# Optimization experiments

Hardware: AMD Instinct MI355X
Metric: run time of the kernel (lower is better)

The kernel has to match this reference:

```python
import jax, jax.numpy as jnp
import numpy as np

THETA = 10000.0
AXES_DIM = (16, 56, 56)  # sums to head_dim=128
HEADS = 24
HEAD_DIM = 128
EPS = 1e-5


def _pos_embed(ids):
    # ids: (S, n_axes) int -> cos, sin each (S, head_dim//2)
    pos = ids.astype(jnp.float32)
    cos_out, sin_out = [], []
    for i, d in enumerate(AXES_DIM):
        freqs = 1.0 / (THETA ** (jnp.arange(0, d, 2, dtype=jnp.float32) / d))  # (d/2,)
        ang = pos[:, i][:, None] * freqs[None, :]  # (S, d/2)
        cos_out.append(jnp.cos(ang))
        sin_out.append(jnp.sin(ang))
    return jnp.concatenate(cos_out, -1), jnp.concatenate(sin_out, -1)


def _rms_norm(x, w):
    # per-head RMSNorm over last dim (head_dim)
    var = jnp.mean(x * x, axis=-1, keepdims=True)
    return x * jax.lax.rsqrt(var + EPS) * w


def _apply_rope(x, cos, sin):
    # non-neox (interleaved) rotary. x: (B,S,H,D), cos/sin: (S,D/2)
    x1 = x[..., 0::2]
    x2 = x[..., 1::2]
    c = cos[None, :, None, :]
    s = sin[None, :, None, :]
    o1 = x1 * c - x2 * s
    o2 = x2 * c + x1 * s
    return jnp.stack([o1, o2], axis=-1).reshape(x.shape)


def setup_inputs() -> dict:
    key = jax.random.key(0)
    ks = jax.random.split(key, 12)
    B, S_img, S_txt, D = 1, 2048, 512, 3072
    sd = 1.0 / np.sqrt(D)
    return {
        "hidden_states": jax.random.normal(ks[0], (B, S_img, D), jnp.float32),
        "encoder_hidden_states": jax.random.normal(ks[1], (B, S_txt, D), jnp.float32),
        "ids": jax.random.randint(ks[2], (S_txt + S_img, 3), 0, 64, jnp.int32),
        "w_qkv": jax.random.normal(ks[3], (D, 3 * D), jnp.float32) * sd,
        "w_add_qkv": jax.random.normal(ks[4], (D, 3 * D), jnp.float32) * sd,
        "b_add_qkv": jax.random.normal(ks[5], (3 * D,), jnp.float32) * 0.02,
        "w_out": jax.random.normal(ks[6], (D, D), jnp.float32) * sd,
        "b_out": jax.random.normal(ks[7], (D,), jnp.float32) * 0.02,
        "w_add_out": jax.random.normal(ks[8], (D, D), jnp.float32) * sd,
        "b_add_out": jax.random.normal(ks[9], (D,), jnp.float32) * 0.02,
        "norm_q_w": jnp.ones((HEAD_DIM,), jnp.float32),
        "norm_k_w": jnp.ones((HEAD_DIM,), jnp.float32),
        "norm_add_q_w": jnp.ones((HEAD_DIM,), jnp.float32),
        "norm_add_k_w": jnp.ones((HEAD_DIM,), jnp.float32),
    }


def reference(hidden_states, encoder_hidden_states, ids, w_qkv, w_add_qkv,
              b_add_qkv, w_out, b_out, w_add_out, b_add_out,
              norm_q_w, norm_k_w, norm_add_q_w, norm_add_k_w):
    B, S_img, D = hidden_states.shape
    S_txt = encoder_hidden_states.shape[1]
    H, Dh = HEADS, HEAD_DIM

    # fused QKV projections
    qkv = hidden_states @ w_qkv  # (B, S_img, 3D)
    q, k, v = jnp.split(qkv, 3, axis=-1)
    q = _rms_norm(q.reshape(B, S_img, H, Dh), norm_q_w)
    k = _rms_norm(k.reshape(B, S_img, H, Dh), norm_k_w)
    v = v.reshape(B, S_img, H, Dh)

    eqkv = encoder_hidden_states @ w_add_qkv + b_add_qkv
    eq, ek, ev = jnp.split(eqkv, 3, axis=-1)
    eq = _rms_norm(eq.reshape(B, S_txt, H, Dh), norm_add_q_w)
    ek = _rms_norm(ek.reshape(B, S_txt, H, Dh), norm_add_k_w)
    ev = ev.reshape(B, S_txt, H, Dh)

    # joint sequence: text first, then image
    q = jnp.concatenate([eq, q], axis=1)
    k = jnp.concatenate([ek, k], axis=1)
    v = jnp.concatenate([ev, v], axis=1)

    # multi-axis RoPE over joint positions
    cos, sin = _pos_embed(ids)  # (S_txt+S_img, Dh/2)
    q = _apply_rope(q, cos, sin)
    k = _apply_rope(k, cos, sin)

    # scaled dot-product attention (non-causal)
    scale = 1.0 / np.sqrt(Dh)
    scores = jnp.einsum("bqhd,bkhd->bhqk", q, k) * scale
    probs = jax.nn.softmax(scores, axis=-1)
    attn = jnp.einsum("bhqk,bkhd->bqhd", probs, v)
    attn = attn.reshape(B, S_txt + S_img, H * Dh)

    enc_out = attn[:, :S_txt] @ w_add_out + b_add_out
    img_out = attn[:, S_txt:] @ w_out + b_out
    return img_out, enc_out
```

## Files before the change

kernel.cpp:

```cpp
#include <hip/hip_runtime.h>

typedef __attribute__((ext_vector_type(8))) short short8;
typedef __attribute__((ext_vector_type(4))) short short4v;
typedef __attribute__((ext_vector_type(4))) float floatx4;

__device__ __forceinline__ float b2f(short b) {
  union { unsigned u; float f; } v; v.u = ((unsigned)(unsigned short)b) << 16; return v.f;
}
__device__ __forceinline__ short f2b(float f) {
  union { float f; unsigned u; } v; v.f = f;
  return (short)((v.u + 0x7fffu + ((v.u >> 16) & 1u)) >> 16);
}
__device__ __forceinline__ unsigned cvtpk(float lo, float hi) {
  unsigned r;
  asm("v_cvt_pk_bf16_f32 %0, %1, %2" : "=v"(r) : "v"(lo), "v"(hi));
  return r;
}
__device__ __forceinline__ float loadf(const void* p, size_t i, bool f32) {
  return f32 ? ((const float*)p)[i] : b2f(((const short*)p)[i]);
}
__device__ __forceinline__ short8 load8(const void* p, size_t i, bool f32) {
  if (f32) {
    const float* fp = (const float*)p + i;
    float4 a = *(const float4*)fp;
    float4 b = *(const float4*)(fp + 4);
    short8 r;
    r[0] = f2b(a.x); r[1] = f2b(a.y); r[2] = f2b(a.z); r[3] = f2b(a.w);
    r[4] = f2b(b.x); r[5] = f2b(b.y); r[6] = f2b(b.z); r[7] = f2b(b.w);
    return r;
  }
  return *(const short8*)((const short*)p + i);
}

__device__ __forceinline__ void gload16(const short* g, short* l) {
  __builtin_amdgcn_global_load_lds(
      (const __attribute__((address_space(1))) unsigned int*)g,
      (__attribute__((address_space(3))) unsigned int*)l, 16, 0, 0);
}

__global__ void detect_dtype(const unsigned short* __restrict__ w, int* __restrict__ flag) {
  __shared__ int cnt;
  if (threadIdx.x == 0) cnt = 0;
  __syncthreads();
  int bad = 0;
  for (int i = threadIdx.x; i < 4096; i += 256) {
    int e = (w[i] >> 7) & 0xFF;
    if (e >= 0xC8) bad++;
  }
  atomicAdd(&cnt, bad);
  __syncthreads();
  if (threadIdx.x == 0) *flag = (cnt > 64) ? 1 : 0;
}

__global__ __launch_bounds__(256)
void cvt_bf16_2(const void* __restrict__ srcA, long n8A,
                const void* __restrict__ srcB, long n8B,
                short* __restrict__ dst, const int* __restrict__ dflag) {
  const bool f32 = (*dflag != 0);
  const long n8 = n8A + n8B;
  long stride = (long)gridDim.x * 256;
  for (long i = (long)blockIdx.x * 256 + threadIdx.x; i < n8; i += stride) {
    const void* s; long e;
    if (i < n8A) { s = srcA; e = i * 8; } else { s = srcB; e = (i - n8A) * 8; }
    if (f32) {
      const float* fp = (const float*)s + e;
      float4 a = *(const float4*)fp;
      float4 b = *(const float4*)(fp + 4);
      short8 r;
      r[0] = f2b(a.x); r[1] = f2b(a.y); r[2] = f2b(a.z); r[3] = f2b(a.w);
      r[4] = f2b(b.x); r[5] = f2b(b.y); r[6] = f2b(b.z); r[7] = f2b(b.w);
      *(short8*)(dst + i * 8) = r;
    } else {
      *(short8*)(dst + i * 8) = *(const short8*)((const short*)s + e);
    }
  }
}

__global__ __launch_bounds__(256)
void cvt_tw(const void* __restrict__ wq, short* __restrict__ wqd,
            const void* __restrict__ waq, short* __restrict__ waqd,
            const void* __restrict__ wo, short* __restrict__ wod,
            const void* __restrict__ wao, short* __restrict__ waod,
            const int* __restrict__ dflag) {
  __shared__ short st[64][72];
  const bool f32 = (*dflag != 0);
  const int K = 3072;
  int b = blockIdx.x;
  const void* src; short* dst; int N, n0, k0;
  if (b < 13824) {
    src = (b < 6912) ? wq : waq;
    dst = (b < 6912) ? wqd : waqd;
    int rem = b % 6912;
    N = 9216; n0 = (rem % 144) << 6; k0 = (rem / 144) << 6;
  } else {
    b -= 13824;
    src = (b < 2304) ? wo : wao;
    dst = (b < 2304) ? wod : waod;
    int rem = b % 2304;
    N = 3072; n0 = (rem % 48) << 6; k0 = (rem / 48) << 6;
  }
  const int c4 = threadIdx.x & 15;
  const int rq = threadIdx.x >> 4;
#pragma unroll
  for (int r = 0; r < 4; ++r) {
    int k = r * 16 + rq;
    int n = c4 * 4;
    short v0, v1, v2, v3;
    if (f32) {
      const float* sp = (const float*)src + (size_t)(k0 + k) * N + n0 + n;
      float4 f = *(const float4*)sp;
      v0 = f2b(f.x); v1 = f2b(f.y); v2 = f2b(f.z); v3 = f2b(f.w);
    } else {
      const short* sp = (const short*)src + (size_t)(k0 + k) * N + n0 + n;
      short4v s = *(const short4v*)sp;
      v0 = s[0]; v1 = s[1]; v2 = s[2]; v3 = s[3];
    }
    st[n + 0][k] = v0; st[n + 1][k] = v1; st[n + 2][k] = v2; st[n + 3][k] = v3;
  }
  __syncthreads();
  const int n = threadIdx.x >> 2;
  const int kc = (threadIdx.x & 3) << 4;
  short8 a = *(const short8*)(&st[n][kc]);
  short8 bb = *(const short8*)(&st[n][kc + 8]);
  short* dp = dst + (size_t)(n0 + n) * K + k0 + kc;
  *(short8*)(dp) = a;
  *(short8*)(dp + 8) = bb;
}

__global__ __launch_bounds__(256, 2)
void gemm_bt(const void* __restrict__ A, int a_row0,
             const void* __restrict__ B, const void* __restrict__ bias,
             void* __restrict__ C, int c_row0, int N, int K,
             const int* __restrict__ dflag, int aIn, int cOut) {
  __shared__ short As[128 * 32];
  __shared__ short Bs[128 * 32];
  const bool f32 = (*dflag != 0);
  const bool a32 = aIn && f32;
  const bool c32 = cOut && f32;
  const int tid = threadIdx.x;
  const int lane = tid & 63, w = tid >> 6;
  const int wm = w & 1, wn = w >> 1;
  const int qg = lane >> 4, l16 = lane & 15;
  const int m0 = blockIdx.y << 7, n0 = blockIdx.x << 7;

  const int arow = tid >> 2, ak = (tid & 3) << 3;
  const int brow = tid >> 4, bc = (tid & 15) << 3;
  const int rot = tid & 15;

  floatx4 acc[4][4];
#pragma unroll
  for (int i = 0; i < 4; ++i)
#pragma unroll
    for (int j = 0; j < 4; ++j) acc[i][j] = (floatx4){0.f, 0.f, 0.f, 0.f};

  for (int k0 = 0; k0 < K; k0 += 32) {
    __syncthreads();
#pragma unroll
    for (int j = 0; j < 2; ++j) {
      short8 av = load8(A, (size_t)(a_row0 + m0 + j * 64 + arow) * K + (k0 + ak), a32);
      *(short8*)(As + (j * 64 + arow) * 32 + ak) = av;
      int kr = j * 16 + brow;
      short8 bv = load8(B, (size_t)(k0 + kr) * N + (n0 + bc), f32);
      int kq = kr >> 3, kj = kr & 7;
#pragma unroll
      for (int s = 0; s < 8; ++s) {
        int u = (s + rot) & 7;
        int n = bc + u;
        Bs[(n << 5) + ((kq ^ (n & 3)) << 3) + kj] = bv[u];
      }
    }
    __syncthreads();
    short8 a[4];
#pragma unroll
    for (int mi = 0; mi < 4; ++mi)
      a[mi] = *(const short8*)(As + (wm * 64 + mi * 16 + l16) * 32 + qg * 8);
#pragma unroll
    for (int ni = 0; ni < 4; ++ni) {
      int n = wn * 64 + ni * 16 + l16;
      short8 b = *(const short8*)(Bs + (n << 5) + ((qg ^ (n & 3)) << 3));
#pragma unroll
      for (int mi = 0; mi < 4; ++mi)
        acc[mi][ni] = __builtin_amdgcn_mfma_f32_16x16x32_bf16(a[mi], b, acc[mi][ni], 0, 0, 0);
    }
  }
#pragma unroll
  for (int ni = 0; ni < 4; ++ni) {
    int col = n0 + wn * 64 + ni * 16 + l16;
    float bv = bias ? loadf(bias, col, f32) : 0.0f;
#pragma unroll
    for (int mi = 0; mi < 4; ++mi) {
      int row = m0 + wm * 64 + mi * 16 + qg * 4;
#pragma unroll
      for (int r = 0; r < 4; ++r) {
        size_t idx = (size_t)(c_row0 + row + r) * N + col;
        float val = acc[mi][ni][r] + bv;
        if (c32) ((float*)C)[idx] = val;
        else     ((short*)C)[idx] = f2b(val);
      }
    }
  }
}

__global__ __launch_bounds__(256, 2)
void gemm_bf2(const short* __restrict__ A,
              const short* __restrict__ BTa, const void* __restrict__ biasa,
              int a0a, int c0a, int nYa,
              const short* __restrict__ BTb, const void* __restrict__ biasb,
              int a0b, int c0b,
              void* __restrict__ C, int N, int K,
              const int* __restrict__ dflag, int cOut) {
  __shared__ short Ls[3 * 8192 + 3 * 4096];
#define ASB(b) (Ls + (b) * 8192)
#define BSB(b) (Ls + 24576 + (b) * 4096)
  const bool f32 = (*dflag != 0);
  const bool c32 = cOut && f32;
  const int bx = blockIdx.x;
  const int y = blockIdx.y;
  const short* BT; const void* bias; int arow0, crow0;
  if (y < nYa) { BT = BTa; bias = biasa; arow0 = a0a + (y << 8); crow0 = c0a + (y << 8); }
  else { int my = y - nYa; BT = BTb; bias = biasb; arow0 = a0b + (my << 8); crow0 = c0b + (my << 8); }
  const int tid = threadIdx.x;
  const int lane = tid & 63, w = tid >> 6;
  const int wm = w & 1, wn = w >> 1;
  const int qg = lane >> 4, l16 = lane & 15;
  const int n0 = bx << 7;
  const int garow = lane >> 2;
  const int gcir = lane & 3;
  const int nk = K >> 5;
  const int swz = (gcir ^ (garow & 3) ^ (garow >> 2)) << 3;
  const short* Abase = A + (size_t)(arow0 + w * 64 + garow) * K + swz;
  const short* Bbase = BT + (size_t)(n0 + w * 32 + garow) * K + swz;
  const int rswz = (l16 & 3) ^ (l16 >> 2);

  floatx4 acc[8][4];
#pragma unroll
  for (int i = 0; i < 8; ++i)
#pragma unroll
    for (int j = 0; j < 4; ++j) acc[i][j] = (floatx4){0.f, 0.f, 0.f, 0.f};

  auto STAGE = [&](int buf, int k0) {
#pragma unroll
    for (int j = 0; j < 4; ++j)
      gload16(Abase + (size_t)j * 16 * K + k0, ASB(buf) + ((w * 4 + j) << 9));
#pragma unroll
    for (int j = 0; j < 2; ++j)
      gload16(Bbase + (size_t)j * 16 * K + k0, BSB(buf) + ((w * 2 + j) << 9));
  };

  STAGE(0, 0);
  if (nk > 1) STAGE(1, 32);

  int cb = 0;
  for (int t = 0; t < nk; ++t) {
    if (t + 1 < nk) {
      asm volatile("s_waitcnt vmcnt(6) lgkmcnt(0)" ::: "memory");
    } else {
      asm volatile("s_waitcnt vmcnt(0) lgkmcnt(0)" ::: "memory");
    }
    __builtin_amdgcn_s_barrier();
    if (t + 2 < nk) {
      int sb = (cb == 0) ? 2 : cb - 1;
      STAGE(sb, (t + 2) << 5);
    }
    short8 a[8], b[4];
#pragma unroll
    for (int mi = 0; mi < 8; ++mi) {
      int ra = wm * 128 + mi * 16 + l16;
      a[mi] = *(const short8*)(ASB(cb) + (ra << 5) + ((qg ^ rswz) << 3));
    }
#pragma unroll
    for (int ni = 0; ni < 4; ++ni) {
      int n = wn * 64 + ni * 16 + l16;
      b[ni] = *(const short8*)(BSB(cb) + (n << 5) + ((qg ^ rswz) << 3));
    }
    __builtin_amdgcn_s_setprio(1);
#pragma unroll
    for (int ni = 0; ni < 4; ++ni)
#pragma unroll
      for (int mi = 0; mi < 8; ++mi)
        acc[mi][ni] = __builtin_amdgcn_mfma_f32_16x16x32_bf16(a[mi], b[ni], acc[mi][ni], 0, 0, 0);
    __builtin_amdgcn_s_setprio(0);
    cb = (cb == 2) ? 0 : cb + 1;
  }
  __builtin_amdgcn_s_barrier();
  if (!c32) {
    short* wreg = Ls + w * 4096;
#pragma unroll
    for (int half = 0; half < 2; ++half) {
#pragma unroll
      for (int ni = 0; ni < 4; ++ni) {
        float bvv = bias ? loadf(bias, n0 + wn * 64 + ni * 16 + l16, f32) : 0.0f;
#pragma unroll
        for (int mi2 = 0; mi2 < 4; ++mi2)
#pragma unroll
          for (int r = 0; r < 4; ++r)
            wreg[(mi2 * 16 + qg * 4 + r) * 64 + ni * 16 + l16] =
                f2b(acc[half * 4 + mi2][ni][r] + bvv);
      }
      asm volatile("s_waitcnt lgkmcnt(0)" ::: "memory");
#pragma unroll
      for (int j = 0; j < 8; ++j) {
        int row = j * 8 + (lane >> 3);
        int col = (lane & 7) * 8;
        short8 v = *(const short8*)(wreg + row * 64 + col);
        *(short8*)((short*)C + (size_t)(crow0 + wm * 128 + half * 64 + row) * N +
                   n0 + wn * 64 + col) = v;
      }
      asm volatile("s_waitcnt lgkmcnt(0)" ::: "memory");
    }
  } else {
    float* wregf = (float*)(Ls) + w * 2048;
#pragma unroll
    for (int half = 0; half < 2; ++half) {
#pragma unroll
      for (int ch = 0; ch < 2; ++ch) {
#pragma unroll
        for (int nh = 0; nh < 2; ++nh) {
          int ni = ch * 2 + nh;
          float bvv = bias ? loadf(bias, n0 + wn * 64 + ni * 16 + l16, f32) : 0.0f;
#pragma unroll
          for (int mi2 = 0; mi2 < 4; ++mi2)
#pragma unroll
            for (int r = 0; r < 4; ++r)
              wregf[(mi2 * 16 + qg * 4 + r) * 32 + nh * 16 + l16] =
                  acc[half * 4 + mi2][ni][r] + bvv;
        }
        asm volatile("s_waitcnt lgkmcnt(0)" ::: "memory");
#pragma unroll
        for (int j = 0; j < 8; ++j) {
          int row = j * 8 + (lane >> 3);
          int c4 = (lane & 7) * 4;
          float4 v = *(const float4*)(wregf + row * 32 + c4);
          *(float4*)((float*)C + (size_t)(crow0 + wm * 128 + half * 64 + row) * N +
                     n0 + wn * 64 + ch * 32 + c4) = v;
        }
        asm volatile("s_waitcnt lgkmcnt(0)" ::: "memory");
      }
    }
  }
#undef ASB
#undef BSB
}

__global__ __launch_bounds__(256, 3)
void gemm_bf128(const short* __restrict__ A,
                const short* __restrict__ BTa, const void* __restrict__ biasa,
                int a0a, int c0a, int nYa,
                const short* __restrict__ BTb, const void* __restrict__ biasb,
                int a0b, int c0b,
                void* __restrict__ C, int N, int K,
                const int* __restrict__ dflag, int cOut) {
  __shared__ short Ls[6 * 128 * 32];
#define ASB(b) (Ls + (b) * 4096)
#define BSB(b) (Ls + (3 + (b)) * 4096)
  const bool f32 = (*dflag != 0);
  const bool c32 = cOut && f32;
  const int bx = blockIdx.x;
  const int y = blockIdx.y;
  const short* BT; const void* bias; int arow0, crow0;
  if (y < nYa) { BT = BTa; bias = biasa; arow0 = a0a + (y << 7); crow0 = c0a + (y << 7); }
  else { int my = y - nYa; BT = BTb; bias = biasb; arow0 = a0b + (my << 7); crow0 = c0b + (my << 7); }
  const int tid = threadIdx.x;
  const int lane = tid & 63, w = tid >> 6;
  const int wm = w & 1, wn = w >> 1;
  const int qg = lane >> 4, l16 = lane & 15;
  const int n0 = bx << 7;
  const int garow = lane >> 2;
  const int gcir = lane & 3;
  const int nk = K >> 5;
  const int swz = (gcir ^ (garow & 3) ^ (garow >> 2)) << 3;
  const short* Abase = A + (size_t)(arow0 + w * 32 + garow) * K + swz;
  const short* Bbase = BT + (size_t)(n0 + w * 32 + garow) * K + swz;
  const int rswz = (l16 & 3) ^ (l16 >> 2);

  floatx4 acc[4][4];
#pragma unroll
  for (int i = 0; i < 4; ++i)
#pragma unroll
    for (int j = 0; j < 4; ++j) acc[i][j] = (floatx4){0.f, 0.f, 0.f, 0.f};

  auto STAGE = [&](int buf, int k0) {
#pragma unroll
    for (int j = 0; j < 2; ++j) {
      gload16(Abase + (size_t)j * 16 * K + k0, ASB(buf) + ((w * 2 + j) << 9));
      gload16(Bbase + (size_t)j * 16 * K + k0, BSB(buf) + ((w * 2 + j) << 9));
    }
  };

  STAGE(0, 0);
  if (nk > 1) STAGE(1, 32);

  int cb = 0;
  for (int t = 0; t < nk; ++t) {
    if (t + 1 < nk) {
      asm volatile("s_waitcnt vmcnt(4) lgkmcnt(0)" ::: "memory");
    } else {
      asm volatile("s_waitcnt vmcnt(0) lgkmcnt(0)" ::: "memory");
    }
    __builtin_amdgcn_s_barrier();
    if (t + 2 < nk) {
      int sb = (cb == 0) ? 2 : cb - 1;
      STAGE(sb, (t + 2) << 5);
    }
    short8 a[4], b[4];
#pragma unroll
    for (int mi = 0; mi < 4; ++mi) {
      int ra = wm * 64 + mi * 16 + l16;
      a[mi] = *(const short8*)(ASB(cb) + (ra << 5) + ((qg ^ rswz) << 3));
    }
#pragma unroll
    for (int ni = 0; ni < 4; ++ni) {
      int n = wn * 64 + ni * 16 + l16;
      b[ni] = *(const short8*)(BSB(cb) + (n << 5) + ((qg ^ rswz) << 3));
    }
    __builtin_amdgcn_s_setprio(1);
#pragma unroll
    for (int ni = 0; ni < 4; ++ni)
#pragma unroll
      for (int mi = 0; mi < 4; ++mi)
        acc[mi][ni] = __builtin_amdgcn_mfma_f32_16x16x32_bf16(a[mi], b[ni], acc[mi][ni], 0, 0, 0);
    __builtin_amdgcn_s_setprio(0);
    cb = (cb == 2) ? 0 : cb + 1;
  }
  __builtin_amdgcn_s_barrier();
  if (!c32) {
    short* wreg = Ls + w * 4096;
#pragma unroll
    for (int ni = 0; ni < 4; ++ni) {
      float bvv = bias ? loadf(bias, n0 + wn * 64 + ni * 16 + l16, f32) : 0.0f;
#pragma unroll
      for (int mi = 0; mi < 4; ++mi)
#pragma unroll
        for (int r = 0; r < 4; ++r)
          wreg[(mi * 16 + qg * 4 + r) * 64 + ni * 16 + l16] = f2b(acc[mi][ni][r] + bvv);
    }
    asm volatile("s_waitcnt lgkmcnt(0)" ::: "memory");
#pragma unroll
    for (int j = 0; j < 8; ++j) {
      int row = j * 8 + (lane >> 3);
      int col = (lane & 7) * 8;
      short8 v = *(const short8*)(wreg + row * 64 + col);
      *(short8*)((short*)C + (size_t)(crow0 + wm * 64 + row) * N + n0 + wn * 64 + col) = v;
    }
  } else {
    float* wregf = (float*)(Ls) + w * 2048;
#pragma unroll
    for (int half = 0; half < 2; ++half) {
#pragma unroll
      for (int nh = 0; nh < 2; ++nh) {
        int ni = half * 2 + nh;
        float bvv = bias ? loadf(bias, n0 + wn * 64 + ni * 16 + l16, f32) : 0.0f;
#pragma unroll
        for (int mi = 0; mi < 4; ++mi)
#pragma unroll
          for (int r = 0; r < 4; ++r)
            wregf[(mi * 16 + qg * 4 + r) * 32 + nh * 16 + l16] = acc[mi][ni][r] + bvv;
      }
      asm volatile("s_waitcnt lgkmcnt(0)" ::: "memory");
#pragma unroll
      for (int j = 0; j < 8; ++j) {
        int row = j * 8 + (lane >> 3);
        int c4 = (lane & 7) * 4;
        float4 v = *(const float4*)(wregf + row * 32 + c4);
        *(float4*)((float*)C + (size_t)(crow0 + wm * 64 + row) * N + n0 + wn * 64 + half * 32 + c4) = v;
      }
      asm volatile("s_waitcnt lgkmcnt(0)" ::: "memory");
    }
  }
#undef ASB
#undef BSB
}

__global__ __launch_bounds__(512)
void norm_rope(short* __restrict__ qkv, const int* __restrict__ ids,
               const void* __restrict__ nqw, const void* __restrict__ nkw,
               const void* __restrict__ naqw, const void* __restrict__ nakw,
               const int* __restrict__ dflag) {
  const bool f32 = (*dflag != 0);
  const int t = blockIdx.x, wv = threadIdx.x >> 6, lane = threadIdx.x & 63;
  const bool txt = t < 512;
  int p = lane, axis; float expo;
  if (p < 8)       { axis = 0; expo = (float)(2 * p) * (1.0f / 16.0f); }
  else if (p < 36) { axis = 1; expo = (float)(2 * (p - 8)) * (1.0f / 56.0f); }
  else             { axis = 2; expo = (float)(2 * (p - 36)) * (1.0f / 56.0f); }
  float freq = __expf(-expo * 9.210340371976184f);
  float ang = (float)ids[t * 3 + axis] * freq;
  float s, c; sincosf(ang, &s, &c);
  const void* qw = txt ? naqw : nqw;
  const void* kw = txt ? nakw : nkw;
  float w0q = loadf(qw, 2 * lane, f32), w1q = loadf(qw, 2 * lane + 1, f32);
  float w0k = loadf(kw, 2 * lane, f32), w1k = loadf(kw, 2 * lane + 1, f32);
  const float QS = 0.08838834764831845f * 1.4426950408889634f;
#pragma unroll
  for (int i = 0; i < 3; ++i) {
    int h = wv + 8 * i;
    short* qp = qkv + (size_t)t * 9216 + h * 128 + 2 * lane;
    short* kp = qp + 3072;
    union { unsigned u; short sh[2]; } qv, kv;
    qv.u = *(const unsigned*)qp;
    kv.u = *(const unsigned*)kp;
    float q0 = b2f(qv.sh[0]), q1 = b2f(qv.sh[1]);
    float k0 = b2f(kv.sh[0]), k1 = b2f(kv.sh[1]);
    float sq = q0 * q0 + q1 * q1, sk = k0 * k0 + k1 * k1;
#pragma unroll
    for (int o = 1; o < 64; o <<= 1) { sq += __shfl_xor(sq, o); sk += __shfl_xor(sk, o); }
    float rq = rsqrtf(sq * (1.0f / 128.0f) + 1e-5f);
    float rk = rsqrtf(sk * (1.0f / 128.0f) + 1e-5f);
    float qn0 = q0 * rq * w0q, qn1 = q1 * rq * w1q;
    float kn0 = k0 * rk * w0k, kn1 = k1 * rk * w1k;
    float qo0 = qn0 * c - qn1 * s, qo1 = qn1 * c + qn0 * s;
    float ko0 = kn0 * c - kn1 * s, ko1 = kn1 * c + kn0 * s;
    union { unsigned u; short sh[2]; } qo, ko;
    qo.sh[0] = f2b(qo0 * QS);
    qo.sh[1] = f2b(qo1 * QS);
    ko.sh[0] = f2b(ko0); ko.sh[1] = f2b(ko1);
    *(unsigned*)qp = qo.u;
    *(unsigned*)kp = ko.u;
  }
}

__global__ __launch_bounds__(512, 2)
void attn_fa(const short* __restrict__ qkv, short* __restrict__ attn) {
  __shared__ short KVs[2][128 * 128];
  __shared__ short Pw[8][512];
  const int wgid = blockIdx.x;
  const int xcd = wgid & 7, slot = wgid >> 3;
  const int h = xcd * 3 + slot / 20;
  const int qt = slot % 20;
  const int tid = threadIdx.x, lane = tid & 63, w = tid >> 6;
  const int qg = lane >> 4, l16 = lane & 15;
  const int lr = lane >> 4, lc = lane & 15;
  const int q0 = qt << 7;
  const int sc = tid & 15;
  const int srow5 = (tid >> 4) & 15, half = tid >> 8;

  const short* Qg  = qkv + (size_t)q0 * 9216 + h * 128;
  const short* Kg0 = qkv + 3072 + h * 128;
  const short* Vg0 = qkv + 6144 + h * 128;

#pragma unroll
  for (int j = 0; j < 4; ++j) {
    int row = j * 32 + w * 4 + lr;
    gload16(Kg0 + (size_t)row * 9216 + ((lc ^ (row & 7)) << 3),
            &KVs[0][(j * 32 + w * 4) * 128]);
  }
  short8 aq[4];
#pragma unroll
  for (int kc = 0; kc < 4; ++kc)
    aq[kc] = *(const short8*)(Qg + (size_t)(w * 16 + l16) * 9216 + kc * 32 + qg * 8);
  short8 vr[4];
#pragma unroll
  for (int j = 0; j < 4; ++j) {
    int row = half * 64 + j * 16 + srow5;
    vr[j] = *(const short8*)(Vg0 + (size_t)row * 9216 + sc * 8);
  }
  asm volatile("s_waitcnt vmcnt(8) lgkmcnt(0)" ::: "memory");
  __builtin_amdgcn_s_barrier();

  floatx4 acc_o[8];
#pragma unroll
  for (int nd = 0; nd < 8; ++nd) acc_o[nd] = (floatx4){0.f, 0.f, 0.f, 0.f};
  float m_i[4], l_i[4];
#pragma unroll
  for (int r = 0; r < 4; ++r) { m_i[r] = -1e30f; l_i[r] = 0.0f; }

  for (int kt = 0; kt < 20; ++kt) {
    const int cb = kt & 1;
    asm volatile("s_waitcnt vmcnt(4) lgkmcnt(0)" ::: "memory");
    __builtin_amdgcn_s_barrier();
    if (kt < 19) {
      const short* Kg = qkv + ((size_t)(kt + 1) * 128) * 9216 + 3072 + h * 128;
#pragma unroll
      for (int j = 0; j < 4; ++j) {
        int row = j * 32 + w * 4 + lr;
        gload16(Kg + (size_t)row * 9216 + ((lc ^ (row & 7)) << 3),
                &KVs[1 - cb][(j * 32 + w * 4) * 128]);
      }
    }
    floatx4 acc_s[8];
#pragma unroll
    for (int ni = 0; ni < 8; ++ni) acc_s[ni] = (floatx4){0.f, 0.f, 0.f, 0.f};
    __builtin_amdgcn_s_setprio(1);
#pragma unroll
    for (int kc = 0; kc < 4; ++kc) {
#pragma unroll
      for (int ni = 0; ni < 8; ++ni) {
        int row = ni * 16 + l16;
        short8 b = *(const short8*)(&KVs[cb][row * 128 + (((kc * 4 + qg) ^ (row & 7)) << 3)]);
        acc_s[ni] = __builtin_amdgcn_mfma_f32_16x16x32_bf16(aq[kc], b, acc_s[ni], 0, 0, 0);
      }
    }
    __builtin_amdgcn_s_setprio(0);
    float mxv[4];
    bool need = false;
#pragma unroll
    for (int r = 0; r < 4; ++r) {
      float mx = acc_s[0][r];
#pragma unroll
      for (int ni = 1; ni < 8; ++ni) mx = fmaxf(mx, acc_s[ni][r]);
      mx = fmaxf(mx, __shfl_xor(mx, 1));
      mx = fmaxf(mx, __shfl_xor(mx, 2));
      mx = fmaxf(mx, __shfl_xor(mx, 4));
      mx = fmaxf(mx, __shfl_xor(mx, 8));
      mxv[r] = mx;
      need = need || (mx > m_i[r] + 8.0f);
    }
    if (__ballot(need)) {
#pragma unroll
      for (int r = 0; r < 4; ++r) {
        float mn = fmaxf(m_i[r], mxv[r]);
        float al = __builtin_amdgcn_exp2f(m_i[r] - mn);
        m_i[r] = mn;
        l_i[r] *= al;
#pragma unroll
        for (int nd = 0; nd < 8; ++nd) acc_o[nd][r] *= al;
      }
    }
    unsigned pkr[4][4];
#pragma unroll
    for (int r = 0; r < 4; ++r) {
      float pv[8];
      float rs = 0.f;
#pragma unroll
      for (int ni = 0; ni < 8; ++ni) {
        pv[ni] = __builtin_amdgcn_exp2f(acc_s[ni][r] - m_i[r]);
        rs += pv[ni];
      }
#pragma unroll
      for (int kc = 0; kc < 4; ++kc) pkr[r][kc] = cvtpk(pv[2 * kc], pv[2 * kc + 1]);
      rs += __shfl_xor(rs, 1); rs += __shfl_xor(rs, 2);
      rs += __shfl_xor(rs, 4); rs += __shfl_xor(rs, 8);
      l_i[r] += rs;
    }
    asm volatile("s_waitcnt lgkmcnt(0)" ::: "memory");
    __builtin_amdgcn_s_barrier();
#pragma unroll
    for (int u = 0; u < 8; ++u) {
      int d = sc * 8 + u;
      int xr = (d & 7) ^ ((d >> 3) & 7);
#pragma unroll
      for (int jp = 0; jp < 2; ++jp) {
        int kcw = 2 * half + jp;
        int g = kcw * 4 + (srow5 >> 2);
        union { unsigned uu; short sh[2]; } pk;
        pk.sh[0] = vr[2 * jp][u]; pk.sh[1] = vr[2 * jp + 1][u];
        *(unsigned*)(&KVs[cb][d * 128 + ((g ^ xr) << 3) + ((2 * srow5) & 7)]) = pk.uu;
      }
    }
    if (kt < 19) {
      const short* Vg = qkv + ((size_t)(kt + 1) * 128) * 9216 + 6144 + h * 128;
#pragma unroll
      for (int j = 0; j < 4; ++j) {
        int row = half * 64 + j * 16 + srow5;
        vr[j] = *(const short8*)(Vg + (size_t)row * 9216 + sc * 8);
      }
    }
    asm volatile("s_waitcnt lgkmcnt(0)" ::: "memory");
    __builtin_amdgcn_s_barrier();
    __builtin_amdgcn_s_setprio(1);
#pragma unroll
    for (int kc = 0; kc < 4; ++kc) {
#pragma unroll
      for (int r = 0; r < 4; ++r)
        *(unsigned*)(&Pw[w][(qg * 4 + r) * 32 + ((l16 ^ (qg << 2)) << 1)]) = pkr[r][kc];
      short8 ap = *(const short8*)(&Pw[w][l16 * 32 + ((qg ^ (l16 >> 2)) << 3)]);
#pragma unroll
      for (int nd = 0; nd < 8; ++nd) {
        int d = nd * 16 + l16;
        int chn = (kc * 4 + qg) ^ (d & 7) ^ ((d >> 3) & 7);
        short8 b = *(const short8*)(&KVs[cb][d * 128 + (chn << 3)]);
        acc_o[nd] = __builtin_amdgcn_mfma_f32_16x16x32_bf16(ap, b, acc_o[nd], 0, 0, 0);
      }
    }
    __builtin_amdgcn_s_setprio(0);
  }
  asm volatile("s_waitcnt lgkmcnt(0)" ::: "memory");
  __builtin_amdgcn_s_barrier();
  short* Es = &KVs[0][0];
  float inv[4];
#pragma unroll
  for (int r = 0; r < 4; ++r) inv[r] = 1.0f / l_i[r];
#pragma unroll
  for (int nd = 0; nd < 8; ++nd)
#pragma unroll
    for (int r = 0; r < 4; ++r) {
      int row = w * 16 + qg * 4 + r;
      Es[row * 128 + nd * 16 + l16] = f2b(acc_o[nd][r] * inv[r]);
    }
  asm volatile("s_waitcnt lgkmcnt(0)" ::: "memory");
#pragma unroll
  for (int j = 0; j < 4; ++j) {
    int rrow = w * 16 + j * 4 + qg;
    short8 vv = *(const short8*)(Es + rrow * 128 + l16 * 8);
    *(short8*)(attn + (size_t)(q0 + rrow) * 3072 + h * 128 + l16 * 8) = vv;
  }
}

extern "C" void kernel_launch(void* const* d_in, const int* in_sizes, int n_in,
                              void* d_out, int out_size, void* d_ws, size_t ws_size,
                              hipStream_t stream) {
  (void)in_sizes; (void)n_in; (void)out_size;
  const void* hidden    = d_in[0];
  const void* enc       = d_in[1];
  const int*  ids       = (const int*)d_in[2];
  const void* w_qkv     = d_in[3];
  const void* w_add_qkv = d_in[4];
  const void* b_add_qkv = d_in[5];
  const void* w_out     = d_in[6];
  const void* b_out     = d_in[7];
  const void* w_add_out = d_in[8];
  const void* b_add_out = d_in[9];
  const void* nqw  = d_in[10];
  const void* nkw  = d_in[11];
  const void* naqw = d_in[12];
  const void* nakw = d_in[13];

  int*   dflag = (int*)d_ws;
  short* qkv   = (short*)((char*)d_ws + 256);
  short* attnB = qkv + (size_t)2560 * 9216;

  short* pool  = attnB + (size_t)2560 * 3072;
  const long n_hid  = 2048L * 3072;
  const long n_enc  = 512L * 3072;
  const long n_wqkv = 3072L * 9216;
  const long n_wout = 3072L * 3072;
  short* xb   = pool;
  short* wqb  = xb + n_enc + n_hid;
  short* waqb = wqb + n_wqkv;
  short* wob  = waqb + n_wqkv;
  short* waob = wob + n_wout;
  const size_t REQ = 256 + 2 * ((size_t)2560 * 9216 + (size_t)2560 * 3072 +
                                n_hid + n_enc + 2 * n_wqkv + 2 * n_wout);

  detect_dtype<<<1, 256, 0, stream>>>((const unsigned short*)w_qkv, dflag);

  if (ws_size >= REQ) {
    cvt_bf16_2<<<1024, 256, 0, stream>>>(enc, n_enc / 8, hidden, n_hid / 8, xb, dflag);
    cvt_tw<<<dim3(18432), 256, 0, stream>>>(w_qkv, wqb, w_add_qkv, waqb,
                                            w_out, wob, w_add_out, waob, dflag);

    gemm_bf2<<<dim3(72, 10), 256, 0, stream>>>(
        xb, waqb, b_add_qkv, 0, 0, 2, wqb, nullptr, 512, 512,
        qkv, 9216, 3072, dflag, 0);
    norm_rope<<<dim3(2560), 512, 0, stream>>>(qkv, ids, nqw, nkw, naqw, nakw, dflag);
    attn_fa<<<dim3(480), 512, 0, stream>>>(qkv, attnB);
    gemm_bf128<<<dim3(24, 20), 256, 0, stream>>>(
        attnB, wob, b_out, 512, 0, 16, waob, b_add_out, 0, 2048,
        d_out, 3072, 3072, dflag, 1);
  } else {
    gemm_bt<<<dim3(72, 4), 256, 0, stream>>>(enc, 0, w_add_qkv, b_add_qkv, qkv, 0, 9216, 3072, dflag, 1, 0);
    gemm_bt<<<dim3(72, 16), 256, 0, stream>>>(hidden, 0, w_qkv, nullptr, qkv, 512, 9216, 3072, dflag, 1, 0);
    norm_rope<<<dim3(2560), 512, 0, stream>>>(qkv, ids, nqw, nkw, naqw, nakw, dflag);
    attn_fa<<<dim3(480), 512, 0, stream>>>(qkv, attnB);
    gemm_bt<<<dim3(24, 16), 256, 0, stream>>>(attnB, 512, w_out, b_out, d_out, 0, 3072, 3072, dflag, 0, 1);
    gemm_bt<<<dim3(24, 4), 256, 0, stream>>>(attnB, 0, w_add_out, b_add_out, d_out, 2048, 3072, 3072, dflag, 0, 1);
  }
}
```

Measured before the change: 785.1 us.

## Fuse RMSNorm and RoPE into QKV GEMM epilogue with precomputed rope table

Moves the per-head RMSNorm and interleaved RoPE from a separate norm_rope kernel into the epilogue of the QKV GEMM. Row sums of squares are reduced across the two N-warps through shared memory, and rotation partners are exchanged with lane shuffles. A small rope_tab kernel precomputes cos/sin into the attention buffer before the GEMM. This removes a full read-modify-write pass over Q and K. In exchange it adds an extra barrier, table loads and shuffles to the GEMM epilogue, and relies on the 128-wide N tiles lining up with head boundaries.

```diff
diff --git a/kernel.cpp b/kernel.cpp
--- a/kernel.cpp
+++ b/kernel.cpp
@@ -127,6 +127,20 @@
   *(short8*)(dp + 8) = bb;
 }
 
+__global__ __launch_bounds__(256)
+void rope_tab(const int* __restrict__ ids, float2* __restrict__ rt) {
+  int idx = blockIdx.x * 256 + threadIdx.x;
+  int t = idx >> 6, p = idx & 63;
+  int axis; float expo;
+  if (p < 8)       { axis = 0; expo = (float)(2 * p) * (1.0f / 16.0f); }
+  else if (p < 36) { axis = 1; expo = (float)(2 * (p - 8)) * (1.0f / 56.0f); }
+  else             { axis = 2; expo = (float)(2 * (p - 36)) * (1.0f / 56.0f); }
+  float freq = __expf(-expo * 9.210340371976184f);
+  float ang = (float)ids[t * 3 + axis] * freq;
+  float s, c; sincosf(ang, &s, &c);
+  rt[idx] = make_float2(c, s);
+}
+
 __global__ __launch_bounds__(256, 2)
 void gemm_bt(const void* __restrict__ A, int a_row0,
              const void* __restrict__ B, const void* __restrict__ bias,
@@ -201,6 +215,54 @@
   }
 }
 
+__global__ __launch_bounds__(512)
+void norm_rope(short* __restrict__ qkv, const int* __restrict__ ids,
+               const void* __restrict__ nqw, const void* __restrict__ nkw,
+               const void* __restrict__ naqw, const void* __restrict__ nakw,
+               const int* __restrict__ dflag) {
+  const bool f32 = (*dflag != 0);
+  const int t = blockIdx.x, wv = threadIdx.x >> 6, lane = threadIdx.x & 63;
+  const bool txt = t < 512;
+  int p = lane, axis; float expo;
+  if (p < 8)       { axis = 0; expo = (float)(2 * p) * (1.0f / 16.0f); }
+  else if (p < 36) { axis = 1; expo = (float)(2 * (p - 8)) * (1.0f / 56.0f); }
+  else             { axis = 2; expo = (float)(2 * (p - 36)) * (1.0f / 56.0f); }
+  float freq = __expf(-expo * 9.210340371976184f);
+  float ang = (float)ids[t * 3 + axis] * freq;
+  float s, c; sincosf(ang, &s, &c);
+  const void* qw = txt ? naqw : nqw;
+  const void* kw = txt ? nakw : nkw;
+  float w0q = loadf(qw, 2 * lane, f32), w1q = loadf(qw, 2 * lane + 1, f32);
+  float w0k = loadf(kw, 2 * lane, f32), w1k = loadf(kw, 2 * lane + 1, f32);
+  const float QS = 0.08838834764831845f * 1.4426950408889634f;
+#pragma unroll
+  for (int i = 0; i < 3; ++i) {
+    int h = wv + 8 * i;
+    short* qp = qkv + (size_t)t * 9216 + h * 128 + 2 * lane;
+    short* kp = qp + 3072;
+    union { unsigned u; short sh[2]; } qv, kv;
+    qv.u = *(const unsigned*)qp;
+    kv.u = *(const unsigned*)kp;
+    float q0 = b2f(qv.sh[0]), q1 = b2f(qv.sh[1]);
+    float k0 = b2f(kv.sh[0]), k1 = b2f(kv.sh[1]);
+    float sq = q0 * q0 + q1 * q1, sk = k0 * k0 + k1 * k1;
+#pragma unroll
+    for (int o = 1; o < 64; o <<= 1) { sq += __shfl_xor(sq, o); sk += __shfl_xor(sk, o); }
+    float rq = rsqrtf(sq * (1.0f / 128.0f) + 1e-5f);
+    float rk = rsqrtf(sk * (1.0f / 128.0f) + 1e-5f);
+    float qn0 = q0 * rq * w0q, qn1 = q1 * rq * w1q;
+    float kn0 = k0 * rk * w0k, kn1 = k1 * rk * w1k;
+    float qo0 = qn0 * c - qn1 * s, qo1 = qn1 * c + qn0 * s;
+    float ko0 = kn0 * c - kn1 * s, ko1 = kn1 * c + kn0 * s;
+    union { unsigned u; short sh[2]; } qo, ko;
+    qo.sh[0] = f2b(qo0 * QS);
+    qo.sh[1] = f2b(qo1 * QS);
+    ko.sh[0] = f2b(ko0); ko.sh[1] = f2b(ko1);
+    *(unsigned*)qp = qo.u;
+    *(unsigned*)kp = ko.u;
+  }
+}
+
 __global__ __launch_bounds__(256, 2)
 void gemm_bf2(const short* __restrict__ A,
               const short* __restrict__ BTa, const void* __restrict__ biasa,
@@ -208,7 +270,10 @@
               const short* __restrict__ BTb, const void* __restrict__ biasb,
               int a0b, int c0b,
               void* __restrict__ C, int N, int K,
-              const int* __restrict__ dflag, int cOut) {
+              const int* __restrict__ dflag, int cOut,
+              int nrm, const float2* __restrict__ ropetab,
+              const void* __restrict__ nqw, const void* __restrict__ nkw,
+              const void* __restrict__ naqw, const void* __restrict__ nakw) {
   __shared__ short Ls[3 * 8192 + 3 * 4096];
 #define ASB(b) (Ls + (b) * 8192)
 #define BSB(b) (Ls + 24576 + (b) * 4096)
@@ -283,13 +348,70 @@
     cb = (cb == 2) ? 0 : cb + 1;
   }
   __builtin_amdgcn_s_barrier();
+
+  if (nrm) {
+    if (bias) {
+#pragma unroll
+      for (int ni = 0; ni < 4; ++ni) {
+        float bvv = loadf(bias, n0 + wn * 64 + ni * 16 + l16, f32);
+#pragma unroll
+        for (int mi = 0; mi < 8; ++mi)
+#pragma unroll
+          for (int r = 0; r < 4; ++r) acc[mi][ni][r] += bvv;
+      }
+    }
+    if (bx < 48) {
+      float* sums = (float*)(Ls + 20480);
+      const bool isq = (bx < 24);
+      const bool txt = (crow0 < 512);
+      const void* nw = isq ? (txt ? naqw : nqw) : (txt ? nakw : nkw);
+#pragma unroll
+      for (int mi = 0; mi < 8; ++mi) {
+#pragma unroll
+        for (int r = 0; r < 4; ++r) {
+          float ps = 0.f;
+#pragma unroll
+          for (int ni = 0; ni < 4; ++ni) { float v = acc[mi][ni][r]; ps += v * v; }
+          ps += __shfl_xor(ps, 1); ps += __shfl_xor(ps, 2);
+          ps += __shfl_xor(ps, 4); ps += __shfl_xor(ps, 8);
+          if (l16 == 0) sums[(wm * 128 + mi * 16 + qg * 4 + r) * 2 + wn] = ps;
+        }
+      }
+      asm volatile("s_waitcnt lgkmcnt(0)" ::: "memory");
+      __builtin_amdgcn_s_barrier();
+      const float QS = 0.08838834764831845f * 1.4426950408889634f;
+      const float scl = isq ? QS : 1.0f;
+#pragma unroll
+      for (int mi = 0; mi < 8; ++mi) {
+#pragma unroll
+        for (int r = 0; r < 4; ++r) {
+          int row = wm * 128 + mi * 16 + qg * 4 + r;
+          float s2 = sums[row * 2] + sums[row * 2 + 1];
+          float rr = rsqrtf(s2 * (1.0f / 128.0f) + 1e-5f);
+          int tt = crow0 + row;
+#pragma unroll
+          for (int ni = 0; ni < 4; ++ni) {
+            int col = wn * 64 + ni * 16 + l16;
+            float wv = loadf(nw, col, f32);
+            float vn = acc[mi][ni][r] * rr * wv;
+            float vp = __shfl_xor(vn, 1);
+            float2 cs = ropetab[tt * 64 + (col >> 1)];
+            float sgn = (col & 1) ? 1.0f : -1.0f;
+            acc[mi][ni][r] = (vn * cs.x + sgn * vp * cs.y) * scl;
+          }
+        }
+      }
+    }
+  }
+
+  const void* biasS = nrm ? nullptr : bias;
   if (!c32) {
     short* wreg = Ls + w * 4096;
 #pragma unroll
     for (int half = 0; half < 2; ++half) {
 #pragma unroll
       for (int ni = 0; ni < 4; ++ni) {
-        float bvv = bias ? loadf(bias, n0 + wn * 64 + ni * 16 + l16, f32) : 0.0f;
+        float bvv = biasS ? loadf(biasS, n0 + wn * 64 + ni * 16 + l16, f32) : 0.0f;
 #pragma unroll
         for (int mi2 = 0; mi2 < 4; ++mi2)
 #pragma unroll
@@ -317,7 +439,7 @@
 #pragma unroll
         for (int nh = 0; nh < 2; ++nh) {
           int ni = ch * 2 + nh;
-          float bvv = bias ? loadf(bias, n0 + wn * 64 + ni * 16 + l16, f32) : 0.0f;
+          float bvv = biasS ? loadf(biasS, n0 + wn * 64 + ni * 16 + l16, f32) : 0.0f;
 #pragma unroll
           for (int mi2 = 0; mi2 < 4; ++mi2)
 #pragma unroll
@@ -471,54 +593,6 @@
 #undef BSB
 }
 
-__global__ __launch_bounds__(512)
-void norm_rope(short* __restrict__ qkv, const int* __restrict__ ids,
-               const void* __restrict__ nqw, const void* __restrict__ nkw,
-               const void* __restrict__ naqw, const void* __restrict__ nakw,
-               const int* __restrict__ dflag) {
-  const bool f32 = (*dflag != 0);
-  const int t = blockIdx.x, wv = threadIdx.x >> 6, lane = threadIdx.x & 63;
-  const bool txt = t < 512;
-  int p = lane, axis; float expo;
-  if (p < 8)       { axis = 0; expo = (float)(2 * p) * (1.0f / 16.0f); }
-  else if (p < 36) { axis = 1; expo = (float)(2 * (p - 8)) * (1.0f / 56.0f); }
-  else             { axis = 2; expo = (float)(2 * (p - 36)) * (1.0f / 56.0f); }
-  float freq = __expf(-expo * 9.210340371976184f);
-  float ang = (float)ids[t * 3 + axis] * freq;
-  float s, c; sincosf(ang, &s, &c);
-  const void* qw = txt ? naqw : nqw;
-  const void* kw = txt ? nakw : nkw;
-  float w0q = loadf(qw, 2 * lane, f32), w1q = loadf(qw, 2 * lane + 1, f32);
-  float w0k = loadf(kw, 2 * lane, f32), w1k = loadf(kw, 2 * lane + 1, f32);
-  const float QS = 0.08838834764831845f * 1.4426950408889634f;
-#pragma unroll
-  for (int i = 0; i < 3; ++i) {
-    int h = wv + 8 * i;
-    short* qp = qkv + (size_t)t * 9216 + h * 128 + 2 * lane;
-    short* kp = qp + 3072;
-    union { unsigned u; short sh[2]; } qv, kv;
-    qv.u = *(const unsigned*)qp;
-    kv.u = *(const unsigned*)kp;
-    float q0 = b2f(qv.sh[0]), q1 = b2f(qv.sh[1]);
-    float k0 = b2f(kv.sh[0]), k1 = b2f(kv.sh[1]);
-    float sq = q0 * q0 + q1 * q1, sk = k0 * k0 + k1 * k1;
-#pragma unroll
-    for (int o = 1; o < 64; o <<= 1) { sq += __shfl_xor(sq, o); sk += __shfl_xor(sk, o); }
-    float rq = rsqrtf(sq * (1.0f / 128.0f) + 1e-5f);
-    float rk = rsqrtf(sk * (1.0f / 128.0f) + 1e-5f);
-    float qn0 = q0 * rq * w0q, qn1 = q1 * rq * w1q;
-    float kn0 = k0 * rk * w0k, kn1 = k1 * rk * w1k;
-    float qo0 = qn0 * c - qn1 * s, qo1 = qn1 * c + qn0 * s;
-    float ko0 = kn0 * c - kn1 * s, ko1 = kn1 * c + kn0 * s;
-    union { unsigned u; short sh[2]; } qo, ko;
-    qo.sh[0] = f2b(qo0 * QS);
-    qo.sh[1] = f2b(qo1 * QS);
-    ko.sh[0] = f2b(ko0); ko.sh[1] = f2b(ko1);
-    *(unsigned*)qp = qo.u;
-    *(unsigned*)kp = ko.u;
-  }
-}
-
 __global__ __launch_bounds__(512, 2)
 void attn_fa(const short* __restrict__ qkv, short* __restrict__ attn) {
   __shared__ short KVs[2][128 * 128];
@@ -732,17 +806,20 @@
   const size_t REQ = 256 + 2 * ((size_t)2560 * 9216 + (size_t)2560 * 3072 +
                                 n_hid + n_enc + 2 * n_wqkv + 2 * n_wout);
 
+  float2* rtab = (float2*)attnB;
+
   detect_dtype<<<1, 256, 0, stream>>>((const unsigned short*)w_qkv, dflag);
 
   if (ws_size >= REQ) {
     cvt_bf16_2<<<1024, 256, 0, stream>>>(enc, n_enc / 8, hidden, n_hid / 8, xb, dflag);
     cvt_tw<<<dim3(18432), 256, 0, stream>>>(w_qkv, wqb, w_add_qkv, waqb,
                                             w_out, wob, w_add_out, waob, dflag);
+    rope_tab<<<dim3(640), 256, 0, stream>>>(ids, rtab);
 
     gemm_bf2<<<dim3(72, 10), 256, 0, stream>>>(
         xb, waqb, b_add_qkv, 0, 0, 2, wqb, nullptr, 512, 512,
-        qkv, 9216, 3072, dflag, 0);
-    norm_rope<<<dim3(2560), 512, 0, stream>>>(qkv, ids, nqw, nkw, naqw, nakw, dflag);
+        qkv, 9216, 3072, dflag, 0,
+        1, rtab, nqw, nkw, naqw, nakw);
     attn_fa<<<dim3(480), 512, 0, stream>>>(qkv, attnB);
     gemm_bf128<<<dim3(24, 20), 256, 0, stream>>>(
         attnB, wob, b_out, 512, 0, 16, waob, b_add_out, 0, 2048,
```

After: 911.2 us. +16.1%, slower.
